# Kernel optimization log

Hardware: AMD Instinct MI355X
Metric: run time of the kernel (lower is better)

## Reference

```python
import jax, jax.numpy as jnp
import numpy as np

N_NODES = 50000
N_EDGES = 800000
D = 128
N_GRAPHS = 64


def setup_inputs() -> dict:
    key = jax.random.key(0)
    ks = jax.random.split(key, 10)
    x = jax.random.normal(ks[0], (N_NODES, D), dtype=jnp.float32)
    edge_weight = jax.random.uniform(ks[1], (N_EDGES,), dtype=jnp.float32)
    W1 = jax.random.normal(ks[2], (D, D), dtype=jnp.float32) / np.sqrt(D)
    b1 = jax.random.normal(ks[3], (D,), dtype=jnp.float32) * 0.01
    W2 = jax.random.normal(ks[4], (D, D), dtype=jnp.float32) / np.sqrt(D)
    b2 = jax.random.normal(ks[5], (D,), dtype=jnp.float32) * 0.01
    Wh = jax.random.normal(ks[6], (D, 1), dtype=jnp.float32) / np.sqrt(D)
    bh = jax.random.normal(ks[7], (1,), dtype=jnp.float32) * 0.01
    edge_index = jax.random.randint(ks[8], (2, N_EDGES), 0, N_NODES, dtype=jnp.int64)
    batch = jnp.sort(jax.random.randint(ks[9], (N_NODES,), 0, N_GRAPHS, dtype=jnp.int64))
    return {"x": x, "edge_weight": edge_weight, "W1": W1, "b1": b1,
            "W2": W2, "b2": b2, "Wh": Wh, "bh": bh,
            "edge_index": edge_index, "batch": batch}


def reference(x, edge_weight, W1, b1, W2, b2, Wh, bh, edge_index, batch):
    N = x.shape[0]
    # --- GCN normalization with self-loops (computed once; shared by layers) ---
    row, col = edge_index[0], edge_index[1]
    loop = jnp.arange(N, dtype=edge_index.dtype)
    row2 = jnp.concatenate([row, loop])   # source nodes
    col2 = jnp.concatenate([col, loop])   # target nodes
    ew2 = jnp.concatenate([edge_weight, jnp.ones((N,), dtype=x.dtype)])
    deg = jax.ops.segment_sum(ew2, col2, num_segments=N)
    dinv = jnp.where(deg > 0, jax.lax.rsqrt(deg), 0.0)
    norm = dinv[row2] * ew2 * dinv[col2]  # [E+N]

    def gcn_conv(h, W, b):
        h = h @ W                                   # [N, D_out]
        msg = norm[:, None] * h[row2]               # gather + scale, [E+N, D_out]
        return jax.ops.segment_sum(msg, col2, num_segments=N) + b

    # dropout is identity in eval mode
    h = jax.nn.relu(gcn_conv(x, W1, b1))
    h = jax.nn.relu(gcn_conv(h, W2, b2))

    # --- global mean pool over graphs ---
    counts = jax.ops.segment_sum(jnp.ones((N,), dtype=h.dtype), batch, num_segments=N_GRAPHS)
    pooled = jax.ops.segment_sum(h, batch, num_segments=N_GRAPHS)
    pooled = pooled / jnp.maximum(counts, 1.0)[:, None]
    return pooled @ Wh + bh
```

## Files before the change

### kernel.cpp

```cpp
#include <hip/hip_runtime.h>
#include <hip/hip_bf16.h>
#include <hip/hip_fp16.h>

#define N_NODES  50000
#define N_EDGES  800000
#define D        128
#define N_GRAPHS 64
#define CAP      64
#define EW_SCALE 1048576.0f
#define NB_GEMM1 391
#define NB_FILL  3125

typedef _Float16 half8 __attribute__((ext_vector_type(8)));
typedef float   float4v __attribute__((ext_vector_type(4)));

__device__ __forceinline__ float2 h2f(unsigned int u) {
    __half2 h = *reinterpret_cast<__half2*>(&u);
    return __half22float2(h);
}
__device__ __forceinline__ unsigned int f2h(float a, float b) {
    __half2 h = __floats2half2_rn(a, b);
    return *reinterpret_cast<unsigned int*>(&h);
}
__device__ __forceinline__ float hu2f(unsigned short u) {
    __half_raw hr; hr.x = u;
    return __half2float(__half(hr));
}

__global__ __launch_bounds__(256) void fused_gemm1_fill(const float* __restrict__ X,
                                                        const float* __restrict__ W,
                                                        __half* __restrict__ Yh,
                                                        const int* __restrict__ ei,
                                                        const float* __restrict__ ew,
                                                        unsigned long long* __restrict__ packed,
                                                        unsigned int* __restrict__ bucket) {
    __shared__ float XT[32 * 128];
    __shared__ float Ws[32 * 128];

    if (blockIdx.x >= NB_GEMM1) {
        int e = (blockIdx.x - NB_GEMM1) * 256 + threadIdx.x;
        if (e >= N_EDGES) return;
        int r = ei[e];
        int c = ei[N_EDGES + e];
        float w = ew[e];
        unsigned long long add = (1ULL << 40) | (unsigned long long)(unsigned)(w * EW_SCALE + 0.5f);
        unsigned long long old = atomicAdd(&packed[c], add);
        unsigned pos = (unsigned)(old >> 40);
        if (pos < CAP) {
            unsigned short wh = __half_as_ushort(__float2half_rn(w));
            bucket[(size_t)c * CAP + pos] = (unsigned)r | ((unsigned)wh << 16);
        }
        return;
    }

    const int tid  = threadIdx.x;
    const int row0 = blockIdx.x * 128;
    const int tr = tid >> 4, tc = tid & 15;
    float acc[8][8] = {};

    for (int kt = 0; kt < 4; kt++) {
        const int kbase = kt * 32;
        {
            const float4* src = (const float4*)(W + kbase * 128);
            float4* dst = (float4*)Ws;
            for (int i = tid; i < 1024; i += 256) dst[i] = src[i];
        }
        {
            int r  = tid >> 1;
            int rr = row0 + r; if (rr >= N_NODES) rr = N_NODES - 1;
            int k0 = (tid & 1) * 16;
            const float4* src = (const float4*)(X + (size_t)rr * 128 + kbase + k0);
#pragma unroll
            for (int i = 0; i < 4; i++) {
                float4 v = src[i];
                int k = k0 + i * 4;
                XT[(k + 0) * 128 + r] = v.x;
                XT[(k + 1) * 128 + r] = v.y;
                XT[(k + 2) * 128 + r] = v.z;
                XT[(k + 3) * 128 + r] = v.w;
            }
        }
        __syncthreads();
#pragma unroll 4
        for (int k = 0; k < 32; k++) {
            float xs[8], ws[8];
            *(float4*)&xs[0] = *(const float4*)(XT + k * 128 + tr * 8);
            *(float4*)&xs[4] = *(const float4*)(XT + k * 128 + tr * 8 + 4);
            *(float4*)&ws[0] = *(const float4*)(Ws + k * 128 + tc * 8);
            *(float4*)&ws[4] = *(const float4*)(Ws + k * 128 + tc * 8 + 4);
#pragma unroll
            for (int i = 0; i < 8; i++)
#pragma unroll
                for (int j = 0; j < 8; j++)
                    acc[i][j] += xs[i] * ws[j];
        }
        __syncthreads();
    }
#pragma unroll
    for (int i = 0; i < 8; i++) {
        int r = row0 + tr * 8 + i;
        if (r < N_NODES) {
            uint4 p;
            p.x = f2h(acc[i][0], acc[i][1]);
            p.y = f2h(acc[i][2], acc[i][3]);
            p.z = f2h(acc[i][4], acc[i][5]);
            p.w = f2h(acc[i][6], acc[i][7]);
            *(uint4*)(Yh + (size_t)r * 128 + tc * 8) = p;
        }
    }
}

__global__ void dinv_gstart_kernel(const unsigned long long* __restrict__ packed,
                                   int* __restrict__ cnt, float* __restrict__ dinv,
                                   const int* __restrict__ batch, int* __restrict__ gstart) {
    int i = blockIdx.x * 256 + threadIdx.x;
    if (i >= N_NODES) return;
    unsigned long long p = packed[i];
    int c = (int)(p >> 40);
    cnt[i] = c < CAP ? c : CAP;
    float deg = 1.0f + (float)(p & 0xFFFFFFFFFFULL) * (1.0f / EW_SCALE);
    dinv[i] = rsqrtf(deg);

    int a = batch[i];
    if (i == 0) {
        for (int g = 0; g <= a; g++) gstart[g] = 0;
    } else {
        int pg = batch[i - 1];
        for (int g = pg + 1; g <= a; g++) gstart[g] = i;
    }
    if (i == N_NODES - 1) {
        for (int g = a + 1; g <= N_GRAPHS; g++) gstart[g] = N_NODES;
    }
}

__global__ __launch_bounds__(256) void scale_kernel(unsigned int* __restrict__ xh,
                                                    const float* __restrict__ dinv) {
    int idx = blockIdx.x * 256 + threadIdx.x;
    float dv = dinv[idx >> 6];
    float2 f = h2f(xh[idx]);
    xh[idx] = f2h(f.x * dv, f.y * dv);
}

__global__ __launch_bounds__(256) void gemm2_mfma(const __half* __restrict__ Xh,
                                                  const float* __restrict__ W,
                                                  const float* __restrict__ dinv,
                                                  __half* __restrict__ Yh) {
    const int wv   = threadIdx.x >> 6;
    const int lane = threadIdx.x & 63;
    const int quad = lane >> 4;
    const int l16  = lane & 15;
    const int row0 = blockIdx.x * 64 + wv * 16;
    if (row0 >= N_NODES) return;

    float4v acc[8] = {};

#pragma unroll
    for (int kc = 0; kc < 4; kc++) {
        const int k0 = kc * 32;
        half8 a = *(const half8*)(Xh + (size_t)(row0 + l16) * 128 + k0 + quad * 8);
#pragma unroll
        for (int ct = 0; ct < 8; ct++) {
            const float* wp = W + (size_t)(k0 + quad * 8) * 128 + ct * 16 + l16;
            half8 b;
#pragma unroll
            for (int j = 0; j < 8; j++) b[j] = (_Float16)wp[j * 128];
            acc[ct] = __builtin_amdgcn_mfma_f32_16x16x32_f16(a, b, acc[ct], 0, 0, 0);
        }
    }

#pragma unroll
    for (int r = 0; r < 4; r++) {
        int row = row0 + quad * 4 + r;
        float s = dinv[row];
#pragma unroll
        for (int ct = 0; ct < 8; ct++) {
            Yh[(size_t)row * 128 + ct * 16 + l16] = __float2half_rn(acc[ct][r] * s);
        }
    }
}

__global__ __launch_bounds__(256) void agg_bucket_kernel(const __half* __restrict__ xwh,
                                                         const int* __restrict__ cnt,
                                                         const unsigned int* __restrict__ bucket,
                                                         const float* __restrict__ dinv,
                                                         const float* __restrict__ bias,
                                                         __half* __restrict__ outh) {
    int node = blockIdx.x * 4 + (threadIdx.x >> 6);
    int lane = threadIdx.x & 63;
    const unsigned int* xh = (const unsigned int*)xwh;

    float dv = dinv[node];
    int n = cnt[node];

    unsigned int ehdr = (lane < n) ? bucket[(size_t)node * CAP + lane] : 0u;
    int eh = (int)ehdr;

    float2 xs = h2f(xh[(size_t)node * 64 + lane]);
    float accx = xs.x;
    float accy = xs.y;

    int i = 0;
    for (; i + 3 < n; i += 4) {
        unsigned v0u = (unsigned)__shfl(eh, i);
        unsigned v1u = (unsigned)__shfl(eh, i + 1);
        unsigned v2u = (unsigned)__shfl(eh, i + 2);
        unsigned v3u = (unsigned)__shfl(eh, i + 3);
        int r0 = v0u & 0xFFFF, r1 = v1u & 0xFFFF, r2 = v2u & 0xFFFF, r3 = v3u & 0xFFFF;
        float v0 = hu2f((unsigned short)(v0u >> 16));
        float v1 = hu2f((unsigned short)(v1u >> 16));
        float v2 = hu2f((unsigned short)(v2u >> 16));
        float v3 = hu2f((unsigned short)(v3u >> 16));
        float2 f0 = h2f(xh[(size_t)r0 * 64 + lane]);
        float2 f1 = h2f(xh[(size_t)r1 * 64 + lane]);
        float2 f2 = h2f(xh[(size_t)r2 * 64 + lane]);
        float2 f3 = h2f(xh[(size_t)r3 * 64 + lane]);
        accx += v0 * f0.x + v1 * f1.x + v2 * f2.x + v3 * f3.x;
        accy += v0 * f0.y + v1 * f1.y + v2 * f2.y + v3 * f3.y;
    }
    for (; i < n; i++) {
        unsigned v0u = (unsigned)__shfl(eh, i);
        int r0 = v0u & 0xFFFF;
        float v0 = hu2f((unsigned short)(v0u >> 16));
        float2 f0 = h2f(xh[(size_t)r0 * 64 + lane]);
        accx += v0 * f0.x;
        accy += v0 * f0.y;
    }

    float2 b = ((const float2*)bias)[lane];
    float ox = fmaxf(dv * accx + b.x, 0.0f);
    float oy = fmaxf(dv * accy + b.y, 0.0f);
    ((unsigned int*)outh)[(size_t)node * 64 + lane] = f2h(ox, oy);
}

__global__ __launch_bounds__(256) void agg_head_kernel(const __half* __restrict__ xwh,
                                                       const int* __restrict__ cnt,
                                                       const unsigned int* __restrict__ bucket,
                                                       const float* __restrict__ dinv,
                                                       const float* __restrict__ bias,
                                                       const float* __restrict__ Wh,
                                                       float* __restrict__ nodedot) {
    int node = blockIdx.x * 4 + (threadIdx.x >> 6);
    int lane = threadIdx.x & 63;
    const unsigned int* xh = (const unsigned int*)xwh;

    float dv = dinv[node];
    int n = cnt[node];

    unsigned int ehdr = (lane < n) ? bucket[(size_t)node * CAP + lane] : 0u;
    int eh = (int)ehdr;

    float2 xs = h2f(xh[(size_t)node * 64 + lane]);
    float accx = xs.x;
    float accy = xs.y;

    int i = 0;
    for (; i + 3 < n; i += 4) {
        unsigned v0u = (unsigned)__shfl(eh, i);
        unsigned v1u = (unsigned)__shfl(eh, i + 1);
        unsigned v2u = (unsigned)__shfl(eh, i + 2);
        unsigned v3u = (unsigned)__shfl(eh, i + 3);
        int r0 = v0u & 0xFFFF, r1 = v1u & 0xFFFF, r2 = v2u & 0xFFFF, r3 = v3u & 0xFFFF;
        float v0 = hu2f((unsigned short)(v0u >> 16));
        float v1 = hu2f((unsigned short)(v1u >> 16));
        float v2 = hu2f((unsigned short)(v2u >> 16));
        float v3 = hu2f((unsigned short)(v3u >> 16));
        float2 f0 = h2f(xh[(size_t)r0 * 64 + lane]);
        float2 f1 = h2f(xh[(size_t)r1 * 64 + lane]);
        float2 f2 = h2f(xh[(size_t)r2 * 64 + lane]);
        float2 f3 = h2f(xh[(size_t)r3 * 64 + lane]);
        accx += v0 * f0.x + v1 * f1.x + v2 * f2.x + v3 * f3.x;
        accy += v0 * f0.y + v1 * f1.y + v2 * f2.y + v3 * f3.y;
    }
    for (; i < n; i++) {
        unsigned v0u = (unsigned)__shfl(eh, i);
        int r0 = v0u & 0xFFFF;
        float v0 = hu2f((unsigned short)(v0u >> 16));
        float2 f0 = h2f(xh[(size_t)r0 * 64 + lane]);
        accx += v0 * f0.x;
        accy += v0 * f0.y;
    }

    float2 b = ((const float2*)bias)[lane];
    float hx = fmaxf(dv * accx + b.x, 0.0f);
    float hy = fmaxf(dv * accy + b.y, 0.0f);
    float2 w = ((const float2*)Wh)[lane];
    float s = hx * w.x + hy * w.y;
#pragma unroll
    for (int off = 32; off > 0; off >>= 1) s += __shfl_down(s, off, 64);
    if (lane == 0) nodedot[node] = s;
}

__global__ __launch_bounds__(256) void final2_kernel(const float* __restrict__ nodedot,
                                                     const int* __restrict__ gstart,
                                                     const float* __restrict__ bh,
                                                     float* __restrict__ out) {
    __shared__ float red[256];
    int g = blockIdx.x;
    int a = gstart[g], b = gstart[g + 1];
    float s = 0.0f;
    for (int n = a + threadIdx.x; n < b; n += 256) s += nodedot[n];
    red[threadIdx.x] = s;
    __syncthreads();
#pragma unroll
    for (int off = 128; off > 0; off >>= 1) {
        if (threadIdx.x < off) red[threadIdx.x] += red[threadIdx.x + off];
        __syncthreads();
    }
    if (threadIdx.x == 0)
        out[g] = red[0] / fmaxf((float)(b - a), 1.0f) + bh[0];
}

extern "C" void kernel_launch(void* const* d_in, const int* in_sizes, int n_in,
                              void* d_out, int out_size, void* d_ws, size_t ws_size,
                              hipStream_t stream) {
    const float* x   = (const float*)d_in[0];
    const float* ew  = (const float*)d_in[1];
    const float* W1  = (const float*)d_in[2];
    const float* b1  = (const float*)d_in[3];
    const float* W2  = (const float*)d_in[4];
    const float* b2  = (const float*)d_in[5];
    const float* Wh  = (const float*)d_in[6];
    const float* bh  = (const float*)d_in[7];
    const int*   ei  = (const int*)d_in[8];
    const int*   bat = (const int*)d_in[9];
    float* out = (float*)d_out;

    char* ws = (char*)d_ws;
    __half* bufAh  = (__half*)ws;                         ws += (size_t)N_NODES * D * 2;
    __half* bufBh  = (__half*)ws;                         ws += (size_t)N_NODES * D * 2;
    unsigned int* bucket = (unsigned int*)ws;             ws += (size_t)N_NODES * CAP * 4;
    unsigned long long* packed = (unsigned long long*)ws; ws += (size_t)N_NODES * 8;
    float*  dinv    = (float*)ws;                         ws += (size_t)N_NODES * 4;
    int*    cnt     = (int*)ws;                           ws += (size_t)N_NODES * 4;
    int*    gstart  = (int*)ws;                           ws += (N_GRAPHS + 1) * 4;
    float*  nodedot = (float*)ws;                         ws += (size_t)N_NODES * 4;

    const int nb_nodes = (N_NODES + 255) / 256;
    const int nb_agg   = N_NODES / 4;
    const int nb_scale = N_NODES * 64 / 256;
    const int nb_gemm2 = (N_NODES + 63) / 64;

    hipMemsetAsync(packed, 0, (size_t)N_NODES * 8, stream);

    fused_gemm1_fill<<<NB_GEMM1 + NB_FILL, 256, 0, stream>>>(x, W1, bufAh, ei, ew, packed, bucket);

    dinv_gstart_kernel<<<nb_nodes, 256, 0, stream>>>(packed, cnt, dinv, bat, gstart);
    scale_kernel<<<nb_scale, 256, 0, stream>>>((unsigned int*)bufAh, dinv);

    agg_bucket_kernel<<<nb_agg, 256, 0, stream>>>(bufAh, cnt, bucket, dinv, b1, bufBh);

    gemm2_mfma<<<nb_gemm2, 256, 0, stream>>>(bufBh, W2, dinv, bufAh);
    agg_head_kernel<<<nb_agg, 256, 0, stream>>>(bufAh, cnt, bucket, dinv, b2, Wh, nodedot);

    final2_kernel<<<N_GRAPHS, 256, 0, stream>>>(nodedot, gstart, bh, out);
}
```

Baseline: 228.5 us.

## Fuse dinv with scaling and fold mean-pool head into aggregation

```diff
diff --git a/kernel.cpp b/kernel.cpp
--- a/kernel.cpp
+++ b/kernel.cpp
@@ -10,6 +10,7 @@
 #define EW_SCALE 1048576.0f
 #define NB_GEMM1 391
 #define NB_FILL  3125
+#define NB_AGG   12500
 
 typedef _Float16 half8 __attribute__((ext_vector_type(8)));
 typedef float   float4v __attribute__((ext_vector_type(4)));
@@ -110,33 +111,31 @@
     }
 }
 
-__global__ void dinv_gstart_kernel(const unsigned long long* __restrict__ packed,
-                                   int* __restrict__ cnt, float* __restrict__ dinv,
-                                   const int* __restrict__ batch, int* __restrict__ gstart) {
-    int i = blockIdx.x * 256 + threadIdx.x;
-    if (i >= N_NODES) return;
-    unsigned long long p = packed[i];
-    int c = (int)(p >> 40);
-    cnt[i] = c < CAP ? c : CAP;
-    float deg = 1.0f + (float)(p & 0xFFFFFFFFFFULL) * (1.0f / EW_SCALE);
-    dinv[i] = rsqrtf(deg);
-
-    int a = batch[i];
-    if (i == 0) {
-        for (int g = 0; g <= a; g++) gstart[g] = 0;
-    } else {
-        int pg = batch[i - 1];
-        for (int g = pg + 1; g <= a; g++) gstart[g] = i;
-    }
-    if (i == N_NODES - 1) {
-        for (int g = a + 1; g <= N_GRAPHS; g++) gstart[g] = N_NODES;
-    }
-}
-
-__global__ __launch_bounds__(256) void scale_kernel(unsigned int* __restrict__ xh,
-                                                    const float* __restrict__ dinv) {
-    int idx = blockIdx.x * 256 + threadIdx.x;
-    float dv = dinv[idx >> 6];
+__global__ __launch_bounds__(256) void dinv_scale_kernel(const unsigned long long* __restrict__ packed,
+                                                         int* __restrict__ cnt, float* __restrict__ dinv,
+                                                         const int* __restrict__ batch,
+                                                         int* __restrict__ gstart,
+                                                         unsigned int* __restrict__ xh) {
+    __shared__ float sdv[4];
+    const int node0 = blockIdx.x * 4;
+    const int t = threadIdx.x;
+    if (t < 4) {
+        int node = node0 + t;
+        unsigned long long p = packed[node];
+        int c = (int)(p >> 40);
+        cnt[node] = c < CAP ? c : CAP;
+        float dv = rsqrtf(1.0f + (float)(p & 0xFFFFFFFFFFULL) * (1.0f / EW_SCALE));
+        dinv[node] = dv;
+        sdv[t] = dv;
+        int a = batch[node];
+        int pg = (node == 0) ? -1 : batch[node - 1];
+        for (int g = pg + 1; g <= a; g++) gstart[g] = node;
+        if (node == N_NODES - 1)
+            for (int g = a + 1; g <= N_GRAPHS; g++) gstart[g] = N_NODES;
+    }
+    __syncthreads();
+    float dv = sdv[t >> 6];
+    size_t idx = (size_t)node0 * 64 + t;
     float2 f = h2f(xh[idx]);
     xh[idx] = f2h(f.x * dv, f.y * dv);
 }
@@ -238,7 +237,12 @@
                                                        const float* __restrict__ dinv,
                                                        const float* __restrict__ bias,
                                                        const float* __restrict__ Wh,
-                                                       float* __restrict__ nodedot) {
+                                                       const int* __restrict__ batch,
+                                                       const int* __restrict__ gstart,
+                                                       const float* __restrict__ bh,
+                                                       float* __restrict__ pooled,
+                                                       unsigned int* __restrict__ done,
+                                                       float* __restrict__ out) {
     int node = blockIdx.x * 4 + (threadIdx.x >> 6);
     int lane = threadIdx.x & 63;
     const unsigned int* xh = (const unsigned int*)xwh;
@@ -287,27 +291,31 @@
     float s = hx * w.x + hy * w.y;
 #pragma unroll
     for (int off = 32; off > 0; off >>= 1) s += __shfl_down(s, off, 64);
-    if (lane == 0) nodedot[node] = s;
-}
-
-__global__ __launch_bounds__(256) void final2_kernel(const float* __restrict__ nodedot,
-                                                     const int* __restrict__ gstart,
-                                                     const float* __restrict__ bh,
-                                                     float* __restrict__ out) {
-    __shared__ float red[256];
-    int g = blockIdx.x;
-    int a = gstart[g], b = gstart[g + 1];
-    float s = 0.0f;
-    for (int n = a + threadIdx.x; n < b; n += 256) s += nodedot[n];
-    red[threadIdx.x] = s;
+
+    __shared__ float sdot[4];
+    __shared__ int   sg[4];
+    __shared__ bool  lastFlag;
+    if (lane == 0) { sdot[threadIdx.x >> 6] = s; sg[threadIdx.x >> 6] = batch[node]; }
     __syncthreads();
-#pragma unroll
-    for (int off = 128; off > 0; off >>= 1) {
-        if (threadIdx.x < off) red[threadIdx.x] += red[threadIdx.x + off];
-        __syncthreads();
-    }
-    if (threadIdx.x == 0)
-        out[g] = red[0] / fmaxf((float)(b - a), 1.0f) + bh[0];
+    if (threadIdx.x == 0) {
+        float acc = sdot[0]; int cg = sg[0];
+#pragma unroll
+        for (int k = 1; k < 4; k++) {
+            if (sg[k] == cg) acc += sdot[k];
+            else { atomicAdd(&pooled[cg * 16], acc); cg = sg[k]; acc = sdot[k]; }
+        }
+        atomicAdd(&pooled[cg * 16], acc);
+        __threadfence();
+        unsigned p = atomicAdd(done, 1u);
+        lastFlag = (p == (unsigned)(NB_AGG - 1));
+    }
+    __syncthreads();
+    if (lastFlag && threadIdx.x < N_GRAPHS) {
+        int g = threadIdx.x;
+        float sv = atomicAdd(&pooled[g * 16], 0.0f);
+        int a = gstart[g], bb = gstart[g + 1];
+        out[g] = sv / fmaxf((float)(bb - a), 1.0f) + bh[0];
+    }
 }
 
 extern "C" void kernel_launch(void* const* d_in, const int* in_sizes, int n_in,
@@ -330,27 +338,25 @@
     __half* bufBh  = (__half*)ws;                         ws += (size_t)N_NODES * D * 2;
     unsigned int* bucket = (unsigned int*)ws;             ws += (size_t)N_NODES * CAP * 4;
     unsigned long long* packed = (unsigned long long*)ws; ws += (size_t)N_NODES * 8;
-    float*  dinv    = (float*)ws;                         ws += (size_t)N_NODES * 4;
-    int*    cnt     = (int*)ws;                           ws += (size_t)N_NODES * 4;
-    int*    gstart  = (int*)ws;                           ws += (N_GRAPHS + 1) * 4;
-    float*  nodedot = (float*)ws;                         ws += (size_t)N_NODES * 4;
-
-    const int nb_nodes = (N_NODES + 255) / 256;
-    const int nb_agg   = N_NODES / 4;
-    const int nb_scale = N_NODES * 64 / 256;
+    float*  pooled = (float*)ws;                          ws += (size_t)N_GRAPHS * 16 * 4;
+    unsigned int* done = (unsigned int*)ws;               ws += 16;
+    float*  dinv   = (float*)ws;                          ws += (size_t)N_NODES * 4;
+    int*    cnt    = (int*)ws;                            ws += (size_t)N_NODES * 4;
+    int*    gstart = (int*)ws;                            ws += (N_GRAPHS + 1) * 4;
+
+    const size_t zero_bytes = (size_t)N_NODES * 8 + (size_t)N_GRAPHS * 16 * 4 + 16;
     const int nb_gemm2 = (N_NODES + 63) / 64;
 
-    hipMemsetAsync(packed, 0, (size_t)N_NODES * 8, stream);
+    hipMemsetAsync(packed, 0, zero_bytes, stream);
 
     fused_gemm1_fill<<<NB_GEMM1 + NB_FILL, 256, 0, stream>>>(x, W1, bufAh, ei, ew, packed, bucket);
 
-    dinv_gstart_kernel<<<nb_nodes, 256, 0, stream>>>(packed, cnt, dinv, bat, gstart);
-    scale_kernel<<<nb_scale, 256, 0, stream>>>((unsigned int*)bufAh, dinv);
-
-    agg_bucket_kernel<<<nb_agg, 256, 0, stream>>>(bufAh, cnt, bucket, dinv, b1, bufBh);
+    dinv_scale_kernel<<<NB_AGG, 256, 0, stream>>>(packed, cnt, dinv, bat, gstart,
+                                                  (unsigned int*)bufAh);
+
+    agg_bucket_kernel<<<NB_AGG, 256, 0, stream>>>(bufAh, cnt, bucket, dinv, b1, bufBh);
 
     gemm2_mfma<<<nb_gemm2, 256, 0, stream>>>(bufBh, W2, dinv, bufAh);
-    agg_head_kernel<<<nb_agg, 256, 0, stream>>>(bufAh, cnt, bucket, dinv, b2, Wh, nodedot);
-
-    final2_kernel<<<N_GRAPHS, 256, 0, stream>>>(nodedot, gstart, bh, out);
-}
+    agg_head_kernel<<<NB_AGG, 256, 0, stream>>>(bufAh, cnt, bucket, dinv, b2, Wh,
+                                                bat, gstart, bh, pooled, done, out);
+}
```

New measurement: 509.3 us. 123% more time.

## Fuse layer-1 aggregation with GEMM2 and fold dinv scaling into edge weights

Applied to the files above, without the earlier changes.

```diff
diff --git a/kernel.cpp b/kernel.cpp
--- a/kernel.cpp
+++ b/kernel.cpp
@@ -10,6 +10,7 @@
 #define EW_SCALE 1048576.0f
 #define NB_GEMM1 391
 #define NB_FILL  3125
+#define NB_AGG16 3125
 
 typedef _Float16 half8 __attribute__((ext_vector_type(8)));
 typedef float   float4v __attribute__((ext_vector_type(4)));
@@ -133,58 +134,112 @@
     }
 }
 
-__global__ __launch_bounds__(256) void scale_kernel(unsigned int* __restrict__ xh,
-                                                    const float* __restrict__ dinv) {
-    int idx = blockIdx.x * 256 + threadIdx.x;
-    float dv = dinv[idx >> 6];
-    float2 f = h2f(xh[idx]);
-    xh[idx] = f2h(f.x * dv, f.y * dv);
-}
-
-__global__ __launch_bounds__(256) void gemm2_mfma(const __half* __restrict__ Xh,
-                                                  const float* __restrict__ W,
-                                                  const float* __restrict__ dinv,
-                                                  __half* __restrict__ Yh) {
-    const int wv   = threadIdx.x >> 6;
-    const int lane = threadIdx.x & 63;
-    const int quad = lane >> 4;
-    const int l16  = lane & 15;
-    const int row0 = blockIdx.x * 64 + wv * 16;
-    if (row0 >= N_NODES) return;
-
-    float4v acc[8] = {};
-
-#pragma unroll
-    for (int kc = 0; kc < 4; kc++) {
-        const int k0 = kc * 32;
-        half8 a = *(const half8*)(Xh + (size_t)(row0 + l16) * 128 + k0 + quad * 8);
-#pragma unroll
-        for (int ct = 0; ct < 8; ct++) {
-            const float* wp = W + (size_t)(k0 + quad * 8) * 128 + ct * 16 + l16;
-            half8 b;
-#pragma unroll
-            for (int j = 0; j < 8; j++) b[j] = (_Float16)wp[j * 128];
-            acc[ct] = __builtin_amdgcn_mfma_f32_16x16x32_f16(a, b, acc[ct], 0, 0, 0);
-        }
-    }
-
-#pragma unroll
-    for (int r = 0; r < 4; r++) {
-        int row = row0 + quad * 4 + r;
-        float s = dinv[row];
-#pragma unroll
-        for (int ct = 0; ct < 8; ct++) {
-            Yh[(size_t)row * 128 + ct * 16 + l16] = __float2half_rn(acc[ct][r] * s);
-        }
-    }
-}
-
-__global__ __launch_bounds__(256) void agg_bucket_kernel(const __half* __restrict__ xwh,
+__global__ __launch_bounds__(256) void agg1_gemm2_kernel(const __half* __restrict__ xw1,
                                                          const int* __restrict__ cnt,
                                                          const unsigned int* __restrict__ bucket,
                                                          const float* __restrict__ dinv,
-                                                         const float* __restrict__ bias,
-                                                         __half* __restrict__ outh) {
+                                                         const float* __restrict__ b1,
+                                                         const float* __restrict__ W2,
+                                                         __half* __restrict__ x2) {
+    __shared__ _Float16 sh1[16][136];
+    const int wv   = threadIdx.x >> 6;
+    const int lane = threadIdx.x & 63;
+    const unsigned int* xh = (const unsigned int*)xw1;
+    const int node0 = blockIdx.x * 16;
+
+    float2 bb = ((const float2*)b1)[lane];
+
+#pragma unroll
+    for (int j = 0; j < 4; j++) {
+        int node = node0 + wv * 4 + j;
+        float dv = dinv[node];
+        int n = cnt[node];
+
+        unsigned pk = 0u;
+        if (lane < n) {
+            unsigned eh = bucket[(size_t)node * CAP + lane];
+            float v = hu2f((unsigned short)(eh >> 16)) * dinv[eh & 0xFFFFu];
+            pk = (eh & 0xFFFFu) | ((unsigned)__half_as_ushort(__float2half_rn(v)) << 16);
+        }
+        int pki = (int)pk;
+
+        float2 xs = h2f(xh[(size_t)node * 64 + lane]);
+        float accx = dv * xs.x;
+        float accy = dv * xs.y;
+
+        int i = 0;
+        for (; i + 3 < n; i += 4) {
+            unsigned v0u = (unsigned)__shfl(pki, i);
+            unsigned v1u = (unsigned)__shfl(pki, i + 1);
+            unsigned v2u = (unsigned)__shfl(pki, i + 2);
+            unsigned v3u = (unsigned)__shfl(pki, i + 3);
+            int r0 = v0u & 0xFFFF, r1 = v1u & 0xFFFF, r2 = v2u & 0xFFFF, r3 = v3u & 0xFFFF;
+            float v0 = hu2f((unsigned short)(v0u >> 16));
+            float v1 = hu2f((unsigned short)(v1u >> 16));
+            float v2 = hu2f((unsigned short)(v2u >> 16));
+            float v3 = hu2f((unsigned short)(v3u >> 16));
+            float2 f0 = h2f(xh[(size_t)r0 * 64 + lane]);
+            float2 f1 = h2f(xh[(size_t)r1 * 64 + lane]);
+            float2 f2 = h2f(xh[(size_t)r2 * 64 + lane]);
+            float2 f3 = h2f(xh[(size_t)r3 * 64 + lane]);
+            accx += v0 * f0.x + v1 * f1.x + v2 * f2.x + v3 * f3.x;
+            accy += v0 * f0.y + v1 * f1.y + v2 * f2.y + v3 * f3.y;
+        }
+        for (; i < n; i++) {
+            unsigned v0u = (unsigned)__shfl(pki, i);
+            int r0 = v0u & 0xFFFF;
+            float v0 = hu2f((unsigned short)(v0u >> 16));
+            float2 f0 = h2f(xh[(size_t)r0 * 64 + lane]);
+            accx += v0 * f0.x;
+            accy += v0 * f0.y;
+        }
+
+        float hx = fmaxf(dv * accx + bb.x, 0.0f);
+        float hy = fmaxf(dv * accy + bb.y, 0.0f);
+        int lr = wv * 4 + j;
+        sh1[lr][lane * 2]     = (_Float16)hx;
+        sh1[lr][lane * 2 + 1] = (_Float16)hy;
+    }
+    __syncthreads();
+
+    const int quad = lane >> 4;
+    const int l16  = lane & 15;
+    float4v acc0 = {}, acc1 = {};
+#pragma unroll
+    for (int kc = 0; kc < 4; kc++) {
+        const int k0 = kc * 32;
+        half8 a = *(const half8*)(&sh1[l16][k0 + quad * 8]);
+        {
+            const float* wp = W2 + (size_t)(k0 + quad * 8) * 128 + (wv * 2) * 16 + l16;
+            half8 b;
+#pragma unroll
+            for (int jj = 0; jj < 8; jj++) b[jj] = (_Float16)wp[jj * 128];
+            acc0 = __builtin_amdgcn_mfma_f32_16x16x32_f16(a, b, acc0, 0, 0, 0);
+        }
+        {
+            const float* wp = W2 + (size_t)(k0 + quad * 8) * 128 + (wv * 2 + 1) * 16 + l16;
+            half8 b;
+#pragma unroll
+            for (int jj = 0; jj < 8; jj++) b[jj] = (_Float16)wp[jj * 128];
+            acc1 = __builtin_amdgcn_mfma_f32_16x16x32_f16(a, b, acc1, 0, 0, 0);
+        }
+    }
+#pragma unroll
+    for (int r = 0; r < 4; r++) {
+        int row = node0 + quad * 4 + r;
+        float s = dinv[row];
+        x2[(size_t)row * 128 + (wv * 2) * 16 + l16]     = __float2half_rn(acc0[r] * s);
+        x2[(size_t)row * 128 + (wv * 2 + 1) * 16 + l16] = __float2half_rn(acc1[r] * s);
+    }
+}
+
+__global__ __launch_bounds__(256) void agg_head_kernel(const __half* __restrict__ xwh,
+                                                       const int* __restrict__ cnt,
+                                                       const unsigned int* __restrict__ bucket,
+                                                       const float* __restrict__ dinv,
+                                                       const float* __restrict__ bias,
+                                                       const float* __restrict__ Wh,
+                                                       float* __restrict__ nodedot) {
     int node = blockIdx.x * 4 + (threadIdx.x >> 6);
     int lane = threadIdx.x & 63;
     const unsigned int* xh = (const unsigned int*)xwh;
@@ -227,60 +282,6 @@
     }
 
     float2 b = ((const float2*)bias)[lane];
-    float ox = fmaxf(dv * accx + b.x, 0.0f);
-    float oy = fmaxf(dv * accy + b.y, 0.0f);
-    ((unsigned int*)outh)[(size_t)node * 64 + lane] = f2h(ox, oy);
-}
-
-__global__ __launch_bounds__(256) void agg_head_kernel(const __half* __restrict__ xwh,
-                                                       const int* __restrict__ cnt,
-                                                       const unsigned int* __restrict__ bucket,
-                                                       const float* __restrict__ dinv,
-                                                       const float* __restrict__ bias,
-                                                       const float* __restrict__ Wh,
-                                                       float* __restrict__ nodedot) {
-    int node = blockIdx.x * 4 + (threadIdx.x >> 6);
-    int lane = threadIdx.x & 63;
-    const unsigned int* xh = (const unsigned int*)xwh;
-
-    float dv = dinv[node];
-    int n = cnt[node];
-
-    unsigned int ehdr = (lane < n) ? bucket[(size_t)node * CAP + lane] : 0u;
-    int eh = (int)ehdr;
-
-    float2 xs = h2f(xh[(size_t)node * 64 + lane]);
-    float accx = xs.x;
-    float accy = xs.y;
-
-    int i = 0;
-    for (; i + 3 < n; i += 4) {
-        unsigned v0u = (unsigned)__shfl(eh, i);
-        unsigned v1u = (unsigned)__shfl(eh, i + 1);
-        unsigned v2u = (unsigned)__shfl(eh, i + 2);
-        unsigned v3u = (unsigned)__shfl(eh, i + 3);
-        int r0 = v0u & 0xFFFF, r1 = v1u & 0xFFFF, r2 = v2u & 0xFFFF, r3 = v3u & 0xFFFF;
-        float v0 = hu2f((unsigned short)(v0u >> 16));
-        float v1 = hu2f((unsigned short)(v1u >> 16));
-        float v2 = hu2f((unsigned short)(v2u >> 16));
-        float v3 = hu2f((unsigned short)(v3u >> 16));
-        float2 f0 = h2f(xh[(size_t)r0 * 64 + lane]);
-        float2 f1 = h2f(xh[(size_t)r1 * 64 + lane]);
-        float2 f2 = h2f(xh[(size_t)r2 * 64 + lane]);
-        float2 f3 = h2f(xh[(size_t)r3 * 64 + lane]);
-        accx += v0 * f0.x + v1 * f1.x + v2 * f2.x + v3 * f3.x;
-        accy += v0 * f0.y + v1 * f1.y + v2 * f2.y + v3 * f3.y;
-    }
-    for (; i < n; i++) {
-        unsigned v0u = (unsigned)__shfl(eh, i);
-        int r0 = v0u & 0xFFFF;
-        float v0 = hu2f((unsigned short)(v0u >> 16));
-        float2 f0 = h2f(xh[(size_t)r0 * 64 + lane]);
-        accx += v0 * f0.x;
-        accy += v0 * f0.y;
-    }
-
-    float2 b = ((const float2*)bias)[lane];
     float hx = fmaxf(dv * accx + b.x, 0.0f);
     float hy = fmaxf(dv * accy + b.y, 0.0f);
     float2 w = ((const float2*)Wh)[lane];
@@ -336,21 +337,17 @@
     float*  nodedot = (float*)ws;                         ws += (size_t)N_NODES * 4;
 
     const int nb_nodes = (N_NODES + 255) / 256;
-    const int nb_agg   = N_NODES / 4;
-    const int nb_scale = N_NODES * 64 / 256;
-    const int nb_gemm2 = (N_NODES + 63) / 64;
+    const int nb_agg4  = N_NODES / 4;
 
     hipMemsetAsync(packed, 0, (size_t)N_NODES * 8, stream);
 
     fused_gemm1_fill<<<NB_GEMM1 + NB_FILL, 256, 0, stream>>>(x, W1, bufAh, ei, ew, packed, bucket);
 
     dinv_gstart_kernel<<<nb_nodes, 256, 0, stream>>>(packed, cnt, dinv, bat, gstart);
-    scale_kernel<<<nb_scale, 256, 0, stream>>>((unsigned int*)bufAh, dinv);
-
-    agg_bucket_kernel<<<nb_agg, 256, 0, stream>>>(bufAh, cnt, bucket, dinv, b1, bufBh);
-
-    gemm2_mfma<<<nb_gemm2, 256, 0, stream>>>(bufBh, W2, dinv, bufAh);
-    agg_head_kernel<<<nb_agg, 256, 0, stream>>>(bufAh, cnt, bucket, dinv, b2, Wh, nodedot);
+
+    agg1_gemm2_kernel<<<NB_AGG16, 256, 0, stream>>>(bufAh, cnt, bucket, dinv, b1, W2, bufBh);
+
+    agg_head_kernel<<<nb_agg4, 256, 0, stream>>>(bufBh, cnt, bucket, dinv, b2, Wh, nodedot);
 
     final2_kernel<<<N_GRAPHS, 256, 0, stream>>>(nodedot, gstart, bh, out);
 }
```

After: 230.7 us. Within noise of the previous version (+0.9%).
